# Optimization experiments

Measured on AMD Instinct MI355X. Metric: run time of the kernel, lower is better.

The kernel has to match this reference:

```python
import jax, jax.numpy as jnp
import numpy as np

B, C, H, W = 16, 512, 32, 32
HID = 4 * C


def setup_inputs() -> dict:
    key = jax.random.key(0)
    k_x, k_w1, k_w2 = jax.random.split(key, 3)
    x = jax.random.normal(k_x, (B, C, H, W), dtype=jnp.float32)
    # 1x1 conv weights stored as [out, in] matrices (kernel_size=1)
    w1 = jax.random.normal(k_w1, (HID, C), dtype=jnp.float32) * (1.0 / np.sqrt(C))
    b1 = jnp.zeros((HID,), dtype=jnp.float32)
    w2 = jax.random.normal(k_w2, (C, HID), dtype=jnp.float32) * (1.0 / np.sqrt(HID))
    b2 = jnp.zeros((C,), dtype=jnp.float32)
    return {"x": x, "w1": w1, "b1": b1, "w2": w2, "b2": b2}


def reference(x, w1, b1, w2, b2):
    Bd, Cd, Hd, Wd = x.shape
    scale = Cd ** (-0.5)
    xf = x.reshape(Bd, Cd, Hd * Wd)          # [B, C, N]
    q = jnp.swapaxes(xf, -1, -2)              # [B, N, C]
    # full spatial self-attention: scores [B, N, N]
    attn = jax.nn.softmax(jnp.einsum('bnc,bcm->bnm', q, xf) * scale, axis=-1)
    out = jnp.einsum('bnm,bmc->bnc', attn, q)  # [B, N, C]
    # 1x1-conv FFN applied per spatial position
    h = jax.nn.relu(jnp.einsum('bnc,dc->bnd', out, w1) + b1)   # [B, N, 4C]
    y = jnp.einsum('bnd,cd->bnc', h, w2) + b2                  # [B, N, C]
    y = jnp.swapaxes(y, -1, -2).reshape(Bd, Cd, Hd, Wd)
    return y + x
```

## Files before the change

kernel.cpp:

```cpp
#include <hip/hip_runtime.h>

#define BATCH 16
#define CH    512
#define NSP   1024
#define HIDD  2048

typedef __bf16 bf16x8 __attribute__((ext_vector_type(8)));
typedef float floatx4 __attribute__((ext_vector_type(4)));

__device__ __forceinline__ float bf2f(unsigned short u) {
    union { unsigned int i; float f; } v; v.i = ((unsigned int)u) << 16; return v.f;
}
__device__ __forceinline__ unsigned short f2bf(float f) {
    union { float f; unsigned int i; } v; v.f = f;
    unsigned int i = v.i;
    return (unsigned short)((i + 0x7FFFu + ((i >> 16) & 1u)) >> 16);
}

__device__ __forceinline__ void gload16(const void* g, void* l) {
    __builtin_amdgcn_global_load_lds(
        (__attribute__((address_space(1))) unsigned int*)(g),
        (__attribute__((address_space(3))) unsigned int*)(l),
        16, 0, 0);
}
#define MEMFENCE asm volatile("" ::: "memory")
#define SBARRIER asm volatile("s_barrier" ::: "memory")

template<int EPI, int MAP, int DEPTH>
__global__ __launch_bounds__(256, (DEPTH == 2) ? 3 : 2)
void gemm_bt(const unsigned short* __restrict__ A,
             const unsigned short* __restrict__ Bm,
             void* __restrict__ Cout,
             int Nn, int K,
             long sAb, long sBb, long sCb,
             const float* __restrict__ bias, float scale,
             const float* __restrict__ resid,
             float* __restrict__ aux)
{
    constexpr int NBUF = DEPTH + 1;
    __shared__ unsigned short sA[NBUF][128 * 32];
    __shared__ unsigned short sB[NBUF][128 * 32];
    __shared__ float sInv[128];

    const int tid  = threadIdx.x;
    const int lane = tid & 63;
    const int w    = tid >> 6;
    const int quad = lane >> 4;
    const int l15  = lane & 15;
    const int mw   = (w >> 1) * 64;
    const int nw   = (w & 1) * 64;

    const int F = blockIdx.x;
    int m0, n0, b;
    if constexpr (MAP == 1) {
        const int xcd = F & 7, s = F >> 3;
        b = xcd + ((s >> 5) << 3);
        const int j = s & 31; m0 = (j >> 2) << 7; n0 = (j & 3) << 7;
    } else if constexpr (MAP == 3) {
        const int xcd = F & 7, s = F >> 3;
        b = 0; m0 = (s & 3) << 7; n0 = ((xcd << 4) + (s >> 2)) << 7;
    } else {
        const int xcd = F & 7; int s = F >> 3;
        b = xcd + ((s >= 36) ? 8 : 0);
        if (s >= 36) s -= 36;
        int tm = 0;
        while (s >= 8 - tm) { s -= 8 - tm; tm++; }
        m0 = tm << 7; n0 = (tm + s) << 7;
    }

    if constexpr (EPI == 6) {
        if (tid < 128) {
            const float* p = aux + (size_t)b * NSP * 16
                           + (size_t)(m0 + tid) * 16;
            float s = 0.f;
#pragma unroll
            for (int k = 0; k < 16; k++) s += p[k];
            sInv[tid] = 1.0f / s;
        }
        MEMFENCE;
    }

    A  += (size_t)b * sAb;
    Bm += (size_t)b * sBb;

    const int srow = lane >> 2;
    const int sg   = (lane & 3) ^ ((lane >> 3) & 3);
    const unsigned short* pA = A  + (size_t)(m0 + w * 32 + srow) * K + sg * 8;
    const unsigned short* pB = Bm + (size_t)(n0 + w * 32 + srow) * K + sg * 8;
    const size_t rowskip16 = (size_t)16 * K;
    const int woff = w * 1024;
    const int rslot = ((l15 >> 1) & 3);

    floatx4 acc[4][4];
#pragma unroll
    for (int i = 0; i < 4; i++)
#pragma unroll
        for (int j = 0; j < 4; j++) acc[i][j] = (floatx4){0.f, 0.f, 0.f, 0.f};

    const int nIter = K >> 5;
    const int kLast = K - 32;

#pragma unroll
    for (int d = 0; d < DEPTH; ++d) {
        unsigned short* dA = &sA[d][0] + woff;
        unsigned short* dB = &sB[d][0] + woff;
        gload16(pA + d * 32,             dA);
        gload16(pA + d * 32 + rowskip16, dA + 512);
        gload16(pB + d * 32,             dB);
        gload16(pB + d * 32 + rowskip16, dB + 512);
        MEMFENCE;
    }

    int bcur = 0, bpf = DEPTH;
    for (int it = 0; it < nIter; ++it) {
        if constexpr (DEPTH == 2)
            asm volatile("s_waitcnt vmcnt(4)\n\ts_barrier" ::: "memory");
        else
            asm volatile("s_waitcnt vmcnt(8)\n\ts_barrier" ::: "memory");

        const int kpf = (it + DEPTH) * 32 <= kLast ? (it + DEPTH) * 32 : kLast;
        unsigned short* dA = &sA[0][0] + bpf * 4096 + woff;
        unsigned short* dB = &sB[0][0] + bpf * 4096 + woff;
        gload16(pA + kpf,             dA);
        gload16(pA + kpf + rowskip16, dA + 512);
        gload16(pB + kpf,             dB);
        gload16(pB + kpf + rowskip16, dB + 512);
        MEMFENCE;

        const unsigned short* bufA = &sA[0][0] + bcur * 4096;
        const unsigned short* bufB = &sB[0][0] + bcur * 4096;
        bf16x8 af[4], bfr[4];
#pragma unroll
        for (int mi = 0; mi < 4; mi++)
            af[mi] = *(const bf16x8*)(bufA + (mw + mi * 16 + l15) * 32
                                      + (quad ^ rslot) * 8);
#pragma unroll
        for (int ni = 0; ni < 4; ni++)
            bfr[ni] = *(const bf16x8*)(bufB + (nw + ni * 16 + l15) * 32
                                       + (quad ^ rslot) * 8);
#pragma unroll
        for (int mi = 0; mi < 4; mi++)
#pragma unroll
            for (int ni = 0; ni < 4; ni++)
                acc[mi][ni] = __builtin_amdgcn_mfma_f32_16x16x32_bf16(
                    af[mi], bfr[ni], acc[mi][ni], 0, 0, 0);

        bcur = bcur == NBUF - 1 ? 0 : bcur + 1;
        bpf  = bpf  == NBUF - 1 ? 0 : bpf  + 1;
    }
    asm volatile("s_waitcnt vmcnt(0)" ::: "memory");

    if constexpr (EPI == 4) {
        float* Of = (float*)Cout;
#pragma unroll
        for (int mi = 0; mi < 4; mi++) {
#pragma unroll
            for (int r = 0; r < 4; r++) {
                const int c = m0 + mw + mi * 16 + quad * 4 + r;
                const float bv = bias[c];
#pragma unroll
                for (int ni = 0; ni < 4; ni++) {
                    const int j  = n0 + nw + ni * 16 + l15;
                    const int bb = j >> 10, ns = j & 1023;
                    const size_t a = (size_t)bb * CH * NSP + (size_t)c * NSP + ns;
                    Of[a] = acc[mi][ni][r] + bv + resid[a];
                }
            }
        }
    } else if constexpr (EPI == 5) {
#pragma unroll
        for (int mi = 0; mi < 4; mi++)
#pragma unroll
            for (int ni = 0; ni < 4; ni++)
#pragma unroll
                for (int r = 0; r < 4; r++)
                    acc[mi][ni][r] = __expf(acc[mi][ni][r] * scale);
        {
            const int chunk = (n0 + nw) >> 6;
            float* ps = aux + (size_t)b * NSP * 16;
#pragma unroll
            for (int mi = 0; mi < 4; mi++) {
#pragma unroll
                for (int r = 0; r < 4; r++) {
                    float s = acc[mi][0][r] + acc[mi][1][r]
                            + acc[mi][2][r] + acc[mi][3][r];
                    s += __shfl_xor(s, 1);
                    s += __shfl_xor(s, 2);
                    s += __shfl_xor(s, 4);
                    s += __shfl_xor(s, 8);
                    if (l15 == 0)
                        ps[(size_t)(m0 + mw + mi * 16 + quad * 4 + r) * 16
                           + chunk] = s;
                }
            }
        }
        unsigned short* Cb = (unsigned short*)Cout + (size_t)b * sCb;
#pragma unroll
        for (int mi = 0; mi < 4; mi++) {
#pragma unroll
            for (int r = 0; r < 4; r++) {
                const size_t rowoff =
                    (size_t)(m0 + mw + mi * 16 + quad * 4 + r) * Nn;
#pragma unroll
                for (int ni = 0; ni < 4; ni++)
                    Cb[rowoff + n0 + nw + ni * 16 + l15] =
                        f2bf(acc[mi][ni][r]);
            }
        }
        if constexpr (MAP == 4) {
            if (m0 != n0) {
                const int chunkt = (m0 + mw) >> 6;
                float* ps = aux + (size_t)b * NSP * 16;
#pragma unroll
                for (int ni = 0; ni < 4; ni++) {
                    float s = 0.f;
#pragma unroll
                    for (int mi = 0; mi < 4; mi++)
#pragma unroll
                        for (int r = 0; r < 4; r++) s += acc[mi][ni][r];
                    s += __shfl_xor(s, 16);
                    s += __shfl_xor(s, 32);
                    if (quad == 0)
                        ps[(size_t)(n0 + nw + ni * 16 + l15) * 16 + chunkt] = s;
                }
#pragma unroll
                for (int ni = 0; ni < 4; ni++) {
                    const size_t rowoff =
                        (size_t)(n0 + nw + ni * 16 + l15) * Nn;
#pragma unroll
                    for (int mi = 0; mi < 4; mi++) {
                        ushort4 v;
                        v.x = f2bf(acc[mi][ni][0]);
                        v.y = f2bf(acc[mi][ni][1]);
                        v.z = f2bf(acc[mi][ni][2]);
                        v.w = f2bf(acc[mi][ni][3]);
                        *(ushort4*)(Cb + rowoff + m0 + mw + mi * 16 + quad * 4)
                            = v;
                    }
                }
            }
        }
    } else {
        __syncthreads();
        unsigned short* Cb = (unsigned short*)Cout + (size_t)b * sCb;
#pragma unroll
        for (int mi = 0; mi < 4; mi++) {
#pragma unroll
            for (int r = 0; r < 4; r++) {
                const int lrow = mw + mi * 16 + quad * 4 + r;
                const float iv = sInv[lrow];
                const size_t rowoff = (size_t)(m0 + lrow) * Nn;
#pragma unroll
                for (int ni = 0; ni < 4; ni++)
                    Cb[rowoff + n0 + nw + ni * 16 + l15] =
                        f2bf(acc[mi][ni][r] * iv);
            }
        }
    }
}

__global__ __launch_bounds__(256, 2)
void gemm_final_u2(const unsigned short* __restrict__ A,
                   const unsigned short* __restrict__ Bm,
                   float* __restrict__ Of,
                   const float* __restrict__ bias,
                   const float* __restrict__ resid)
{
    const int K = HIDD;
    __shared__ unsigned short sA[4][128 * 32];
    __shared__ unsigned short sB[4][128 * 32];

    const int tid  = threadIdx.x;
    const int lane = tid & 63;
    const int w    = tid >> 6;
    const int quad = lane >> 4;
    const int l15  = lane & 15;
    const int mw   = (w >> 1) * 64;
    const int nw   = (w & 1) * 64;

    const int F = blockIdx.x;
    const int xcd = F & 7, s = F >> 3;
    const int m0 = (s & 3) << 7;
    const int n0 = ((xcd << 4) + (s >> 2)) << 7;

    const int srow = lane >> 2;
    const int sg   = (lane & 3) ^ ((lane >> 3) & 3);
    const unsigned short* pA = A  + (size_t)(m0 + w * 32 + srow) * K + sg * 8;
    const unsigned short* pB = Bm + (size_t)(n0 + w * 32 + srow) * K + sg * 8;
    const size_t rowskip16 = (size_t)16 * K;
    const int woff = w * 1024;
    const int rslot = ((l15 >> 1) & 3);

    floatx4 acc[4][4];
#pragma unroll
    for (int i = 0; i < 4; i++)
#pragma unroll
        for (int j = 0; j < 4; j++) acc[i][j] = (floatx4){0.f, 0.f, 0.f, 0.f};

    const int kLast = K - 32;

#pragma unroll
    for (int d = 0; d < 4; ++d) {
        unsigned short* dA = &sA[d][0] + woff;
        unsigned short* dB = &sB[d][0] + woff;
        gload16(pA + d * 32,             dA);
        gload16(pA + d * 32 + rowskip16, dA + 512);
        gload16(pB + d * 32,             dB);
        gload16(pB + d * 32 + rowskip16, dB + 512);
        MEMFENCE;
    }

    const int nBody = K >> 6;
    for (int i = 0; i < nBody; ++i) {
        asm volatile("s_waitcnt vmcnt(8)\n\ts_barrier" ::: "memory");

#pragma unroll
        for (int t = 0; t < 2; ++t) {
            const int buf = (2 * i + t) & 3;
            const unsigned short* bufA = &sA[buf][0];
            const unsigned short* bufB = &sB[buf][0];
            bf16x8 af[4], bfr[4];
#pragma unroll
            for (int mi = 0; mi < 4; mi++)
                af[mi] = *(const bf16x8*)(bufA + (mw + mi * 16 + l15) * 32
                                          + (quad ^ rslot) * 8);
#pragma unroll
            for (int ni = 0; ni < 4; ni++)
                bfr[ni] = *(const bf16x8*)(bufB + (nw + ni * 16 + l15) * 32
                                           + (quad ^ rslot) * 8);
#pragma unroll
            for (int mi = 0; mi < 4; mi++)
#pragma unroll
                for (int ni = 0; ni < 4; ni++)
                    acc[mi][ni] = __builtin_amdgcn_mfma_f32_16x16x32_bf16(
                        af[mi], bfr[ni], acc[mi][ni], 0, 0, 0);
        }

        __builtin_amdgcn_s_barrier();
#pragma unroll
        for (int t = 0; t < 2; ++t) {
            const int kt = 2 * i + 4 + t;
            const int kpf = (kt * 32 <= kLast) ? kt * 32 : kLast;
            const int buf = kt & 3;
            unsigned short* dA = &sA[buf][0] + woff;
            unsigned short* dB = &sB[buf][0] + woff;
            gload16(pA + kpf,             dA);
            gload16(pA + kpf + rowskip16, dA + 512);
            gload16(pB + kpf,             dB);
            gload16(pB + kpf + rowskip16, dB + 512);
            MEMFENCE;
        }
    }
    asm volatile("s_waitcnt vmcnt(0)" ::: "memory");

#pragma unroll
    for (int mi = 0; mi < 4; mi++) {
#pragma unroll
        for (int r = 0; r < 4; r++) {
            const int c = m0 + mw + mi * 16 + quad * 4 + r;
            const float bv = bias[c];
#pragma unroll
            for (int ni = 0; ni < 4; ni++) {
                const int j  = n0 + nw + ni * 16 + l15;
                const int bb = j >> 10, ns = j & 1023;
                const size_t a = (size_t)bb * CH * NSP + (size_t)c * NSP + ns;
                Of[a] = acc[mi][ni][r] + bv + resid[a];
            }
        }
    }
}

__global__ __launch_bounds__(512, 1)
void ffn1_8ph(const unsigned short* __restrict__ A,
              const unsigned short* __restrict__ Bm,
              unsigned short* __restrict__ Cout,
              const float* __restrict__ bias)
{
    constexpr int K = CH;
    __shared__ unsigned short sA[2][256 * 64];
    __shared__ unsigned short sB[2][256 * 64];

    const int tid  = threadIdx.x;
    const int lane = tid & 63;
    const int w    = tid >> 6;
    const int wr   = w >> 2;
    const int wc   = w & 3;
    const int quad = lane >> 4;
    const int l15  = lane & 15;
    const int swz8 = (l15 & 7) * 8;

    const int F = blockIdx.x;
    const int xcd = F & 7, s = F >> 3;
    const int m0 = ((xcd << 3) + (s >> 3)) << 8;
    const int n0 = (s & 7) << 8;

    const int srow   = tid >> 3;
    const int schunk = (tid & 7) ^ ((tid >> 3) & 7);
    const unsigned short* pAg = A  + (size_t)(m0 + srow) * K + schunk * 8;
    const unsigned short* pBg = Bm + (size_t)(n0 + srow) * K + schunk * 8;
    const int dRow = w * 8;

#define STAGE_A8(kt, nb) do {                                         \
    unsigned short* d = &sA[nb][0];                                   \
    const unsigned short* g = pAg + (kt) * 64;                        \
    gload16(g,                   d + (dRow      ) * 64);              \
    gload16(g + (size_t) 64 * K, d + (dRow +  64) * 64);              \
    gload16(g + (size_t)128 * K, d + (dRow + 128) * 64);              \
    gload16(g + (size_t)192 * K, d + (dRow + 192) * 64);              \
    MEMFENCE; } while (0)
#define STAGE_B8(kt, nb) do {                                         \
    unsigned short* d = &sB[nb][0];                                   \
    const unsigned short* g = pBg + (kt) * 64;                        \
    gload16(g,                   d + (dRow      ) * 64);              \
    gload16(g + (size_t) 64 * K, d + (dRow +  64) * 64);              \
    gload16(g + (size_t)128 * K, d + (dRow + 128) * 64);              \
    gload16(g + (size_t)192 * K, d + (dRow + 192) * 64);              \
    MEMFENCE; } while (0)

    floatx4 acc[8][4];
#pragma unroll
    for (int i = 0; i < 8; i++)
#pragma unroll
        for (int j = 0; j < 4; j++) acc[i][j] = (floatx4){0.f, 0.f, 0.f, 0.f};

    STAGE_A8(0, 0);
    STAGE_B8(0, 0);
    asm volatile("s_waitcnt vmcnt(0)" ::: "memory");
    SBARRIER;

    bf16x8 af[4][2], bfr[4][2];

    for (int kt = 0; kt < 8; ++kt) {
        const unsigned short* bufA = &sA[kt & 1][0];
        const unsigned short* bufB = &sB[kt & 1][0];
        const int nb = (kt + 1) & 1;
        const bool pf = (kt < 7);

#pragma unroll
        for (int i = 0; i < 4; i++) {
            const unsigned short* r = bufA + (size_t)(wr * 128 + i * 16 + l15) * 64;
            af[i][0] = *(const bf16x8*)(r + ((quad * 8) ^ swz8));
            af[i][1] = *(const bf16x8*)(r + ((32 + quad * 8) ^ swz8));
        }
#pragma unroll
        for (int j = 0; j < 2; j++) {
            const unsigned short* r = bufB + (size_t)(wc * 64 + j * 16 + l15) * 64;
            bfr[j][0] = *(const bf16x8*)(r + ((quad * 8) ^ swz8));
            bfr[j][1] = *(const bf16x8*)(r + ((32 + quad * 8) ^ swz8));
        }
        if (pf) STAGE_A8(kt + 1, nb);
        SBARRIER;
        __builtin_amdgcn_s_setprio(1);
#pragma unroll
        for (int i = 0; i < 4; i++)
#pragma unroll
            for (int j = 0; j < 2; j++)
#pragma unroll
                for (int kk = 0; kk < 2; kk++)
                    acc[i][j] = __builtin_amdgcn_mfma_f32_16x16x32_bf16(
                        af[i][kk], bfr[j][kk], acc[i][j], 0, 0, 0);
        __builtin_amdgcn_s_setprio(0);
        SBARRIER;

#pragma unroll
        for (int j = 0; j < 2; j++) {
            const unsigned short* r = bufB + (size_t)(wc * 64 + (2 + j) * 16 + l15) * 64;
            bfr[2 + j][0] = *(const bf16x8*)(r + ((quad * 8) ^ swz8));
            bfr[2 + j][1] = *(const bf16x8*)(r + ((32 + quad * 8) ^ swz8));
        }
        if (pf) STAGE_B8(kt + 1, nb);
        SBARRIER;
        __builtin_amdgcn_s_setprio(1);
#pragma unroll
        for (int i = 0; i < 4; i++)
#pragma unroll
            for (int j = 0; j < 2; j++)
#pragma unroll
                for (int kk = 0; kk < 2; kk++)
                    acc[i][2 + j] = __builtin_amdgcn_mfma_f32_16x16x32_bf16(
                        af[i][kk], bfr[2 + j][kk], acc[i][2 + j], 0, 0, 0);
        __builtin_amdgcn_s_setprio(0);
        SBARRIER;

#pragma unroll
        for (int i = 0; i < 4; i++) {
            const unsigned short* r = bufA + (size_t)(wr * 128 + 64 + i * 16 + l15) * 64;
            af[i][0] = *(const bf16x8*)(r + ((quad * 8) ^ swz8));
            af[i][1] = *(const bf16x8*)(r + ((32 + quad * 8) ^ swz8));
        }
        SBARRIER;
        __builtin_amdgcn_s_setprio(1);
#pragma unroll
        for (int i = 0; i < 4; i++)
#pragma unroll
            for (int j = 0; j < 2; j++)
#pragma unroll
                for (int kk = 0; kk < 2; kk++)
                    acc[4 + i][2 + j] = __builtin_amdgcn_mfma_f32_16x16x32_bf16(
                        af[i][kk], bfr[2 + j][kk], acc[4 + i][2 + j], 0, 0, 0);
        __builtin_amdgcn_s_setprio(0);
        SBARRIER;

        __builtin_amdgcn_s_setprio(1);
#pragma unroll
        for (int i = 0; i < 4; i++)
#pragma unroll
            for (int j = 0; j < 2; j++)
#pragma unroll
                for (int kk = 0; kk < 2; kk++)
                    acc[4 + i][j] = __builtin_amdgcn_mfma_f32_16x16x32_bf16(
                        af[i][kk], bfr[j][kk], acc[4 + i][j], 0, 0, 0);
        __builtin_amdgcn_s_setprio(0);
        if (pf) {
            asm volatile("s_waitcnt vmcnt(0)" ::: "memory");
            SBARRIER;
        }
    }

    float bv[4];
#pragma unroll
    for (int ni = 0; ni < 4; ni++)
        bv[ni] = bias[n0 + wc * 64 + ni * 16 + l15];
#pragma unroll
    for (int mi = 0; mi < 8; mi++) {
#pragma unroll
        for (int r = 0; r < 4; r++) {
            const size_t rowoff =
                (size_t)(m0 + wr * 128 + mi * 16 + quad * 4 + r) * HIDD;
#pragma unroll
            for (int ni = 0; ni < 4; ni++)
                Cout[rowoff + n0 + wc * 64 + ni * 16 + l15] =
                    f2bf(fmaxf(acc[mi][ni][r] + bv[ni], 0.f));
        }
    }
#undef STAGE_A8
#undef STAGE_B8
}

__global__ __launch_bounds__(256)
void prep_kernel(const float* __restrict__ x,
                 unsigned short* __restrict__ Xbf,
                 unsigned short* __restrict__ XT,
                 const float* __restrict__ w1,
                 unsigned short* __restrict__ W1b,
                 const float* __restrict__ w2,
                 unsigned short* __restrict__ W2b)
{
    const int tx = threadIdx.x, ty = threadIdx.y;
    const int z = blockIdx.z;
    if (z < 16) {
        __shared__ float tile[32][33];
        const int n0 = blockIdx.x * 32, c0 = blockIdx.y * 32, b = z;
        const size_t base = (size_t)b * CH * NSP;
#pragma unroll
        for (int i = ty; i < 32; i += 8) {
            float v = x[base + (size_t)(c0 + i) * NSP + n0 + tx];
            tile[i][tx] = v;
            Xbf[base + (size_t)(c0 + i) * NSP + n0 + tx] = f2bf(v);
        }
        __syncthreads();
        const size_t tbase = (size_t)b * NSP * CH;
#pragma unroll
        for (int i = ty; i < 32; i += 8)
            XT[tbase + (size_t)(n0 + i) * CH + c0 + tx] = f2bf(tile[tx][i]);
    } else {
        const int tid = ty * 32 + tx;
        const int blk = (z - 16) * 512 + blockIdx.y * 32 + blockIdx.x;
        const int i = blk * 256 + tid;
        if (i < HIDD * CH) W1b[i] = f2bf(w1[i]);
        else               W2b[i - HIDD * CH] = f2bf(w2[i - HIDD * CH]);
    }
}

extern "C" void kernel_launch(void* const* d_in, const int* in_sizes, int n_in,
                              void* d_out, int out_size, void* d_ws, size_t ws_size,
                              hipStream_t stream)
{
    const float* x  = (const float*)d_in[0];
    const float* w1 = (const float*)d_in[1];
    const float* b1 = (const float*)d_in[2];
    const float* w2 = (const float*)d_in[3];
    const float* b2 = (const float*)d_in[4];
    float* out = (float*)d_out;

    char* ws = (char*)d_ws;
    unsigned short* Xbf = (unsigned short*)ws; ws += (size_t)BATCH * CH * NSP * 2;
    unsigned short* XT  = (unsigned short*)ws; ws += (size_t)BATCH * NSP * CH * 2;
    unsigned short* W1b = (unsigned short*)ws; ws += (size_t)HIDD * CH * 2;
    unsigned short* W2b = (unsigned short*)ws; ws += (size_t)CH * HIDD * 2;
    unsigned short* P   = (unsigned short*)ws; ws += (size_t)BATCH * NSP * NSP * 2;
    unsigned short* O   = (unsigned short*)ws; ws += (size_t)BATCH * NSP * CH * 2;
    unsigned short* Hb  = (unsigned short*)ws; ws += (size_t)BATCH * NSP * HIDD * 2;
    float*          Ps  = (float*)ws;          ws += (size_t)BATCH * NSP * 16 * 4;

    const dim3 blk(256);

    prep_kernel<<<dim3(32, 16, 32), dim3(32, 8), 0, stream>>>(
        x, Xbf, XT, w1, W1b, w2, W2b);

    gemm_bt<5, 4, 2><<<dim3(576), blk, 0, stream>>>(
        XT, XT, P, NSP, CH,
        (long)NSP * CH, (long)NSP * CH, (long)NSP * NSP, nullptr,
        0.04419417382415922f, nullptr, Ps);

    gemm_bt<6, 1, 2><<<dim3(512), blk, 0, stream>>>(
        P, Xbf, O, CH, NSP,
        (long)NSP * NSP, (long)CH * NSP, (long)NSP * CH, nullptr, 1.f,
        nullptr, Ps);

    ffn1_8ph<<<dim3(512), dim3(512), 0, stream>>>(O, W1b, Hb, b1);

    gemm_final_u2<<<dim3(512), blk, 0, stream>>>(
        W2b, Hb, out, b2, x);
}
```

Measured before the change: 236.2 us.

## Restructure FFN1 GEMM into triple-buffered K=32 pipeline with two-deep prefetch

The first FFN GEMM kernel now uses K-tiles of 32 instead of 64, held in three LDS buffers, and keeps two tiles in flight via a vmcnt(4)-gated wait. This replaces the double-buffered four-phase schedule, which drained all loads with vmcnt(0) every iteration. The aim is to hide global-to-LDS latency better and cut the number of barriers per unit of work. In exchange there are twice as many loop iterations, a smaller 4-way XOR swizzle, and redundant clamped prefetches of tile 15 at the tail.

```diff
diff --git a/kernel.cpp b/kernel.cpp
--- a/kernel.cpp
+++ b/kernel.cpp
@@ -371,14 +371,14 @@
 }
 
 __global__ __launch_bounds__(512, 1)
-void ffn1_8ph(const unsigned short* __restrict__ A,
+void ffn1_c32(const unsigned short* __restrict__ A,
               const unsigned short* __restrict__ Bm,
               unsigned short* __restrict__ Cout,
               const float* __restrict__ bias)
 {
     constexpr int K = CH;
-    __shared__ unsigned short sA[2][256 * 64];
-    __shared__ unsigned short sB[2][256 * 64];
+    __shared__ unsigned short sA[3][256 * 32];
+    __shared__ unsigned short sB[3][256 * 32];
 
     const int tid  = threadIdx.x;
     const int lane = tid & 63;
@@ -387,34 +387,30 @@
     const int wc   = w & 3;
     const int quad = lane >> 4;
     const int l15  = lane & 15;
-    const int swz8 = (l15 & 7) * 8;
+    const int rsw  = l15 & 3;
 
     const int F = blockIdx.x;
     const int xcd = F & 7, s = F >> 3;
     const int m0 = ((xcd << 3) + (s >> 3)) << 8;
     const int n0 = (s & 7) << 8;
 
-    const int srow   = tid >> 3;
-    const int schunk = (tid & 7) ^ ((tid >> 3) & 7);
+    const int srow   = tid >> 2;
+    const int schunk = (tid & 3) ^ ((tid >> 2) & 3);
     const unsigned short* pAg = A  + (size_t)(m0 + srow) * K + schunk * 8;
     const unsigned short* pBg = Bm + (size_t)(n0 + srow) * K + schunk * 8;
-    const int dRow = w * 8;
-
-#define STAGE_A8(kt, nb) do {                                         \
-    unsigned short* d = &sA[nb][0];                                   \
-    const unsigned short* g = pAg + (kt) * 64;                        \
-    gload16(g,                   d + (dRow      ) * 64);              \
-    gload16(g + (size_t) 64 * K, d + (dRow +  64) * 64);              \
-    gload16(g + (size_t)128 * K, d + (dRow + 128) * 64);              \
-    gload16(g + (size_t)192 * K, d + (dRow + 192) * 64);              \
+    const int dOff = w * 512;
+
+#define STAGE_A32(kt, nb) do {                                        \
+    unsigned short* d = &sA[nb][0] + dOff;                            \
+    const unsigned short* g = pAg + (kt) * 32;                        \
+    gload16(g,                   d);                                  \
+    gload16(g + (size_t)128 * K, d + 4096);                           \
     MEMFENCE; } while (0)
-#define STAGE_B8(kt, nb) do {                                         \
-    unsigned short* d = &sB[nb][0];                                   \
-    const unsigned short* g = pBg + (kt) * 64;                        \
-    gload16(g,                   d + (dRow      ) * 64);              \
-    gload16(g + (size_t) 64 * K, d + (dRow +  64) * 64);              \
-    gload16(g + (size_t)128 * K, d + (dRow + 128) * 64);              \
-    gload16(g + (size_t)192 * K, d + (dRow + 192) * 64);              \
+#define STAGE_B32(kt, nb) do {                                        \
+    unsigned short* d = &sB[nb][0] + dOff;                            \
+    const unsigned short* g = pBg + (kt) * 32;                        \
+    gload16(g,                   d);                                  \
+    gload16(g + (size_t)128 * K, d + 4096);                           \
     MEMFENCE; } while (0)
 
     floatx4 acc[8][4];
@@ -423,99 +419,62 @@
 #pragma unroll
         for (int j = 0; j < 4; j++) acc[i][j] = (floatx4){0.f, 0.f, 0.f, 0.f};
 
-    STAGE_A8(0, 0);
-    STAGE_B8(0, 0);
-    asm volatile("s_waitcnt vmcnt(0)" ::: "memory");
-    SBARRIER;
-
-    bf16x8 af[4][2], bfr[4][2];
-
-    for (int kt = 0; kt < 8; ++kt) {
-        const unsigned short* bufA = &sA[kt & 1][0];
-        const unsigned short* bufB = &sB[kt & 1][0];
-        const int nb = (kt + 1) & 1;
-        const bool pf = (kt < 7);
-
-#pragma unroll
-        for (int i = 0; i < 4; i++) {
-            const unsigned short* r = bufA + (size_t)(wr * 128 + i * 16 + l15) * 64;
-            af[i][0] = *(const bf16x8*)(r + ((quad * 8) ^ swz8));
-            af[i][1] = *(const bf16x8*)(r + ((32 + quad * 8) ^ swz8));
-        }
-#pragma unroll
-        for (int j = 0; j < 2; j++) {
-            const unsigned short* r = bufB + (size_t)(wc * 64 + j * 16 + l15) * 64;
-            bfr[j][0] = *(const bf16x8*)(r + ((quad * 8) ^ swz8));
-            bfr[j][1] = *(const bf16x8*)(r + ((32 + quad * 8) ^ swz8));
-        }
-        if (pf) STAGE_A8(kt + 1, nb);
+    STAGE_B32(0, 0);
+    STAGE_A32(0, 0);
+    STAGE_B32(1, 1);
+    STAGE_A32(1, 1);
+
+    int bcur = 0, bpf = 2;
+    for (int kt = 0; kt < 16; ++kt) {
+        asm volatile("s_waitcnt vmcnt(4)\n\ts_barrier" ::: "memory");
+
+        const unsigned short* bufA = &sA[bcur][0];
+        const unsigned short* bufB = &sB[bcur][0];
+        const int kpf = (kt + 2 <= 15) ? kt + 2 : 15;
+
+        bf16x8 af[4], bfr[4];
+#pragma unroll
+        for (int i = 0; i < 4; i++)
+            af[i] = *(const bf16x8*)(bufA
+                     + (size_t)(wr * 128 + i * 16 + l15) * 32
+                     + (quad ^ rsw) * 8);
+#pragma unroll
+        for (int j = 0; j < 4; j++)
+            bfr[j] = *(const bf16x8*)(bufB
+                     + (size_t)(wc * 64 + j * 16 + l15) * 32
+                     + (quad ^ rsw) * 8);
+        STAGE_B32(kpf, bpf);
         SBARRIER;
         __builtin_amdgcn_s_setprio(1);
 #pragma unroll
         for (int i = 0; i < 4; i++)
 #pragma unroll
-            for (int j = 0; j < 2; j++)
-#pragma unroll
-                for (int kk = 0; kk < 2; kk++)
-                    acc[i][j] = __builtin_amdgcn_mfma_f32_16x16x32_bf16(
-                        af[i][kk], bfr[j][kk], acc[i][j], 0, 0, 0);
+            for (int j = 0; j < 4; j++)
+                acc[i][j] = __builtin_amdgcn_mfma_f32_16x16x32_bf16(
+                    af[i], bfr[j], acc[i][j], 0, 0, 0);
         __builtin_amdgcn_s_setprio(0);
         SBARRIER;
 
-#pragma unroll
-        for (int j = 0; j < 2; j++) {
-            const unsigned short* r = bufB + (size_t)(wc * 64 + (2 + j) * 16 + l15) * 64;
-            bfr[2 + j][0] = *(const bf16x8*)(r + ((quad * 8) ^ swz8));
-            bfr[2 + j][1] = *(const bf16x8*)(r + ((32 + quad * 8) ^ swz8));
-        }
-        if (pf) STAGE_B8(kt + 1, nb);
-        SBARRIER;
+        bf16x8 ag[4];
+#pragma unroll
+        for (int i = 0; i < 4; i++)
+            ag[i] = *(const bf16x8*)(bufA
+                     + (size_t)(wr * 128 + 64 + i * 16 + l15) * 32
+                     + (quad ^ rsw) * 8);
+        STAGE_A32(kpf, bpf);
         __builtin_amdgcn_s_setprio(1);
 #pragma unroll
         for (int i = 0; i < 4; i++)
 #pragma unroll
-            for (int j = 0; j < 2; j++)
-#pragma unroll
-                for (int kk = 0; kk < 2; kk++)
-                    acc[i][2 + j] = __builtin_amdgcn_mfma_f32_16x16x32_bf16(
-                        af[i][kk], bfr[2 + j][kk], acc[i][2 + j], 0, 0, 0);
+            for (int j = 0; j < 4; j++)
+                acc[4 + i][j] = __builtin_amdgcn_mfma_f32_16x16x32_bf16(
+                    ag[i], bfr[j], acc[4 + i][j], 0, 0, 0);
         __builtin_amdgcn_s_setprio(0);
-        SBARRIER;
-
-#pragma unroll
-        for (int i = 0; i < 4; i++) {
-            const unsigned short* r = bufA + (size_t)(wr * 128 + 64 + i * 16 + l15) * 64;
-            af[i][0] = *(const bf16x8*)(r + ((quad * 8) ^ swz8));
-            af[i][1] = *(const bf16x8*)(r + ((32 + quad * 8) ^ swz8));
-        }
-        SBARRIER;
-        __builtin_amdgcn_s_setprio(1);
-#pragma unroll
-        for (int i = 0; i < 4; i++)
-#pragma unroll
-            for (int j = 0; j < 2; j++)
-#pragma unroll
-                for (int kk = 0; kk < 2; kk++)
-                    acc[4 + i][2 + j] = __builtin_amdgcn_mfma_f32_16x16x32_bf16(
-                        af[i][kk], bfr[2 + j][kk], acc[4 + i][2 + j], 0, 0, 0);
-        __builtin_amdgcn_s_setprio(0);
-        SBARRIER;
-
-        __builtin_amdgcn_s_setprio(1);
-#pragma unroll
-        for (int i = 0; i < 4; i++)
-#pragma unroll
-            for (int j = 0; j < 2; j++)
-#pragma unroll
-                for (int kk = 0; kk < 2; kk++)
-                    acc[4 + i][j] = __builtin_amdgcn_mfma_f32_16x16x32_bf16(
-                        af[i][kk], bfr[j][kk], acc[4 + i][j], 0, 0, 0);
-        __builtin_amdgcn_s_setprio(0);
-        if (pf) {
-            asm volatile("s_waitcnt vmcnt(0)" ::: "memory");
-            SBARRIER;
-        }
-    }
+
+        bcur = bcur == 2 ? 0 : bcur + 1;
+        bpf  = bpf  == 2 ? 0 : bpf  + 1;
+    }
+    asm volatile("s_waitcnt vmcnt(0)" ::: "memory");
 
     float bv[4];
 #pragma unroll
@@ -533,8 +492,8 @@
                     f2bf(fmaxf(acc[mi][ni][r] + bv[ni], 0.f));
         }
     }
-#undef STAGE_A8
-#undef STAGE_B8
+#undef STAGE_A32
+#undef STAGE_B32
 }
 
 __global__ __launch_bounds__(256)
@@ -608,7 +567,7 @@
         (long)NSP * NSP, (long)CH * NSP, (long)NSP * CH, nullptr, 1.f,
         nullptr, Ps);
 
-    ffn1_8ph<<<dim3(512), dim3(512), 0, stream>>>(O, W1b, Hb, b1);
+    ffn1_c32<<<dim3(512), dim3(512), 0, stream>>>(O, W1b, Hb, b1);
 
     gemm_final_u2<<<dim3(512), blk, 0, stream>>>(
         W2b, Hb, out, b2, x);
```

New measurement: 241.4 us. 2.2% more time.
